# Performance work log

Hardware: AMD Instinct MI355X
Metric: run time of the kernel (lower is better)

The kernel has to match this reference:

```python
import jax, jax.numpy as jnp
import numpy as np

B, S, D, H, W, L, V, FF = 8, 4096, 768, 12, 128, 2, 512, 3072
G_IDX = (0,)


def _ln(x, g, b):
    m = x.mean(-1, keepdims=True)
    v = ((x - m) ** 2).mean(-1, keepdims=True)
    return (x - m) * jax.lax.rsqrt(v + 1e-5) * g + b


def _band_blocks(t, w):
    # t: [B,H,S,Dh] -> key/value blocks [B,H,nb,3w,Dh] (prev/cur/next chunk)
    b, h, s, dh = t.shape
    nb = s // w
    tp = jnp.pad(t, ((0, 0), (0, 0), (w, w), (0, 0))).reshape(b, h, nb + 2, w, dh)
    return jnp.concatenate([tp[:, :, 0:nb], tp[:, :, 1:nb + 1], tp[:, :, 2:nb + 2]], axis=3)


def _longformer_attn(x, att_mask, Wq, bq, Wk, bk, Wv, bv, Wo, bo, w, gidx):
    b, s, d = x.shape
    dh = d // H
    proj = lambda Wm, bm: (x @ Wm.T + bm).reshape(b, s, H, dh).transpose(0, 2, 1, 3)
    q = proj(Wq, bq) / np.float32(np.sqrt(dh))
    k = proj(Wk, bk)
    v = proj(Wv, bv)
    nb = s // w
    qb = q.reshape(b, H, nb, w, dh)
    kb = _band_blocks(k, w)
    vb = _band_blocks(v, w)
    sb = jnp.einsum('bhnqd,bhnkd->bhnqk', qb, kb)  # [B,H,nb,w,3w]
    # window validity: key offset jj relative to query i within chunk
    i = jnp.arange(w)[:, None]
    jj = jnp.arange(3 * w)[None, :]
    allowed = (jj - i >= 0) & (jj - i <= 2 * w)  # [w,3w], |rel pos| <= w
    pos = jnp.arange(nb)[:, None] * w - w + jj  # absolute key positions [nb,3w]
    valid = (pos >= 0) & (pos < s)
    # keys that are global or padded are removed from windowed attention (Longformer)
    key_bias = jnp.where(att_mask != 0, -1e4, 0.0)  # [B,S]
    kbias = jnp.pad(key_bias, ((0, 0), (w, w)), constant_values=-1e9).reshape(b, nb + 2, w)
    kbb = jnp.concatenate([kbias[:, 0:nb], kbias[:, 1:nb + 1], kbias[:, 2:nb + 2]], axis=2)  # [B,nb,3w]
    bias = jnp.where(allowed[None, None] & valid[None, :, None, :], kbb[:, :, None, :], -1e9)
    sb = sb + bias[:, None]  # broadcast over heads
    sb_flat = sb.reshape(b, H, s, 3 * w)
    g = jnp.asarray(gidx)
    ng = g.shape[0]
    kg = k[:, :, g]
    vg = v[:, :, g]
    sg = jnp.einsum('bhsd,bhgd->bhsg', q, kg)  # all queries attend global keys
    probs = jax.nn.softmax(jnp.concatenate([sg, sb_flat], axis=-1), axis=-1)
    pg = probs[..., :ng]
    pb = probs[..., ng:].reshape(b, H, nb, w, 3 * w)
    out = jnp.einsum('bhnqk,bhnkd->bhnqd', pb, vb).reshape(b, H, s, dh)
    out = out + jnp.einsum('bhsg,bhgd->bhsd', pg, vg)
    # global query tokens: full attention over all (non-pad) keys
    qg = q[:, :, g]
    sfull = jnp.einsum('bhgd,bhsd->bhgs', qg, k) + jnp.where(att_mask < 0, -1e4, 0.0)[:, None, None, :]
    og = jnp.einsum('bhgs,bhsd->bhgd', jax.nn.softmax(sfull, axis=-1), v)
    out = out.at[:, :, g].set(og)
    out = out.transpose(0, 2, 1, 3).reshape(b, s, d)
    return out @ Wo.T + bo


def setup_inputs() -> dict:
    key = jax.random.key(0)
    ks = jax.random.split(key, 32)
    sc = 0.02
    inp = {
        'call': jax.random.randint(ks[0], (B, S), 0, V),
        'entry': jax.random.randint(ks[1], (B, S), 0, 2),
        'time': jax.random.randint(ks[2], (B, S), 0, 1000),
        'proc': jax.random.randint(ks[3], (B, S), 0, 64),
        'pid': jax.random.randint(ks[4], (B, S), 0, 64),
        'tid': jax.random.randint(ks[5], (B, S), 0, 64),
        'ret': jax.random.randint(ks[6], (B, S), 0, 2),
        'pad_mask': jnp.zeros((B, S), dtype=bool),
        'chk': 0,
        'emb': jax.random.normal(ks[7], (V, D), jnp.float32) * sc,
        'Wq': jax.random.normal(ks[8], (L, D, D), jnp.float32) * sc,
        'bq': jnp.zeros((L, D), jnp.float32),
        'Wk': jax.random.normal(ks[9], (L, D, D), jnp.float32) * sc,
        'bk': jnp.zeros((L, D), jnp.float32),
        'Wv': jax.random.normal(ks[10], (L, D, D), jnp.float32) * sc,
        'bv': jnp.zeros((L, D), jnp.float32),
        'Wo': jax.random.normal(ks[11], (L, D, D), jnp.float32) * sc,
        'bo': jnp.zeros((L, D), jnp.float32),
        'W1': jax.random.normal(ks[12], (L, FF, D), jnp.float32) * sc,
        'b1': jnp.zeros((L, FF), jnp.float32),
        'W2': jax.random.normal(ks[13], (L, D, FF), jnp.float32) * sc,
        'b2': jnp.zeros((L, D), jnp.float32),
        'g1': jnp.ones((L, D), jnp.float32),
        'beta1': jnp.zeros((L, D), jnp.float32),
        'g2': jnp.ones((L, D), jnp.float32),
        'beta2': jnp.zeros((L, D), jnp.float32),
        'gf': jnp.ones((D,), jnp.float32),
        'betaf': jnp.zeros((D,), jnp.float32),
        'Wc': jax.random.normal(ks[14], (V, D), jnp.float32) * sc,
        'bc': jnp.zeros((V,), jnp.float32),
    }
    return inp


def reference(call, entry, time, proc, pid, tid, ret, pad_mask, chk,
              emb, Wq, bq, Wk, bk, Wv, bv, Wo, bo, W1, b1, W2, b2,
              g1, beta1, g2, beta2, gf, betaf, Wc, bc):
    x = emb[call]  # [B,S,D]; only dim_sys > 0 so embedding == emb_call lookup
    g = jnp.asarray(G_IDX)
    att_mask = jnp.zeros((call.shape[0], call.shape[1]), jnp.float32).at[:, g].set(1e4)
    att_mask = jnp.where(pad_mask, -1e4, att_mask)  # _generate_longformer_mask
    for l in range(L):
        a = _longformer_attn(x, att_mask, Wq[l], bq[l], Wk[l], bk[l], Wv[l], bv[l], Wo[l], bo[l], W, G_IDX)
        x = _ln(x + a, g1[l], beta1[l])
        h = jax.nn.relu(x @ W1[l].T + b1[l]) @ W2[l].T + b2[l]
        x = _ln(x + h, g2[l], beta2[l])
    x = _ln(x, gf, betaf)  # encoder final norm (tfixup=False)
    return x @ Wc.T + bc
```

## Files before the change

kernel.cpp:

```cpp
#include <hip/hip_runtime.h>
#include <hip/hip_bf16.h>
#include <cstddef>
#include <cstdint>

#define Bsz 8
#define Ssz 4096
#define Dsz 768
#define Hh  12
#define Wd  128
#define NBl 32
#define DH  64
#define FFs 3072
#define Vs  512
#define Ls  2
#define GNS 16

typedef __attribute__((ext_vector_type(8))) short short8;
typedef __attribute__((ext_vector_type(4))) float f32x4;

typedef __attribute__((address_space(3))) unsigned short as3_ushort;
typedef __attribute__((address_space(1))) unsigned short as1_ushort;

__device__ inline float b2f(unsigned short u) { union { unsigned int i; float f; } x; x.i = ((unsigned int)u) << 16; return x.f; }
__device__ inline float b2f_lo(unsigned int u) { union { unsigned int i; float f; } x; x.i = (u & 0xffffu) << 16; return x.f; }
__device__ inline float b2f_hi(unsigned int u) { union { unsigned int i; float f; } x; x.i = u & 0xffff0000u; return x.f; }
__device__ inline unsigned short f2bu(float f) {
  __hip_bfloat16 h = __float2bfloat16(f);
  return *reinterpret_cast<unsigned short*>(&h);
}
__device__ inline unsigned int pack2(float lo, float hi) {
  return (unsigned int)f2bu(lo) | ((unsigned int)f2bu(hi) << 16);
}
__device__ inline void glds16(const unsigned short* g, unsigned short* l) {
  __builtin_amdgcn_global_load_lds((const as1_ushort*)g, (as3_ushort*)l, 16, 0, 0);
}

__global__ __launch_bounds__(256) void k_convw(const float* __restrict__ src,
                                               unsigned short* __restrict__ dst, int n) {
  int i8 = (blockIdx.x * 256 + threadIdx.x) * 8;
  if (i8 >= n) return;
  const float4* s4 = reinterpret_cast<const float4*>(src);
  float4 a = s4[i8 >> 2], b = s4[(i8 >> 2) + 1];
  uint4 o;
  o.x = pack2(a.x, a.y); o.y = pack2(a.z, a.w);
  o.z = pack2(b.x, b.y); o.w = pack2(b.z, b.w);
  reinterpret_cast<uint4*>(dst)[i8 >> 3] = o;
}

__global__ __launch_bounds__(256) void k_embed(const int* __restrict__ call,
                                               const float* __restrict__ emb,
                                               unsigned short* __restrict__ x) {
  int idx = blockIdx.x * 256 + threadIdx.x;
  int row = idx / 96;
  int c8  = idx % 96;
  int tok = call[row];
  const float4* s4 = reinterpret_cast<const float4*>(emb + (size_t)tok * Dsz);
  float4 a = s4[c8 * 2], b = s4[c8 * 2 + 1];
  uint4 o;
  o.x = pack2(a.x, a.y); o.y = pack2(a.z, a.w);
  o.z = pack2(b.x, b.y); o.w = pack2(b.z, b.w);
  reinterpret_cast<uint4*>(x)[idx] = o;
}

__global__ __launch_bounds__(256) void k_gemm_lds(
    const unsigned short* __restrict__ A, const unsigned short* __restrict__ Wb,
    const float* __restrict__ bias0, const float* __restrict__ bias1,
    const float* __restrict__ bias2,
    void* __restrict__ o0, void* __restrict__ o1, void* __restrict__ o2,
    int M, int N, int K, int Ng,
    float a0, float a1, float a2, int relu, int out_fp32) {
  __shared__ unsigned short As[128 * 32];
  __shared__ unsigned short Bs[128 * 32];

  const int gx = gridDim.x;
  const int total = gx * (int)gridDim.y;
  const int id = blockIdx.y * gx + blockIdx.x;
  const int swz = (id & 7) * (total >> 3) + (id >> 3);
  const int n0 = (swz % gx) * 128;
  const int m0 = (swz / gx) * 128;

  const int tid  = threadIdx.x;
  const int lane = tid & 63;
  const int wv   = tid >> 6;
  const int wm = wv >> 1, wn = wv & 1;
  const int mr = lane & 15, quad = lane >> 4;

  const int c0 = wv, c1 = wv + 4;
  const int row0 = c0 * 16 + (lane >> 2);
  const int row1 = c1 * 16 + (lane >> 2);
  const int kc0 = (lane & 3) ^ ((row0 >> 1) & 3);
  const int kc1 = (lane & 3) ^ ((row1 >> 1) & 3);
  const unsigned short* gA0 = A  + (size_t)(m0 + row0) * K + kc0 * 8;
  const unsigned short* gA1 = A  + (size_t)(m0 + row1) * K + kc1 * 8;
  const unsigned short* gB0 = Wb + (size_t)(n0 + row0) * K + kc0 * 8;
  const unsigned short* gB1 = Wb + (size_t)(n0 + row1) * K + kc1 * 8;

  int offA[4], offB[4];
#pragma unroll
  for (int mf = 0; mf < 4; mf++) {
    int r = wm * 64 + mf * 16 + mr;
    offA[mf] = r * 32 + ((quad ^ ((r >> 1) & 3)) * 8);
  }
#pragma unroll
  for (int nf = 0; nf < 4; nf++) {
    int r = wn * 64 + nf * 16 + mr;
    offB[nf] = r * 32 + ((quad ^ ((r >> 1) & 3)) * 8);
  }

  f32x4 acc[4][4];
#pragma unroll
  for (int i = 0; i < 4; i++)
#pragma unroll
    for (int j = 0; j < 4; j++) acc[i][j] = (f32x4){0.f, 0.f, 0.f, 0.f};

  for (int k0 = 0; k0 < K; k0 += 32) {
    glds16(gA0 + k0, &As[c0 * 512]);
    glds16(gA1 + k0, &As[c1 * 512]);
    glds16(gB0 + k0, &Bs[c0 * 512]);
    glds16(gB1 + k0, &Bs[c1 * 512]);
    __syncthreads();
    short8 af[4], bf[4];
#pragma unroll
    for (int mf = 0; mf < 4; mf++) af[mf] = *reinterpret_cast<const short8*>(&As[offA[mf]]);
#pragma unroll
    for (int nf = 0; nf < 4; nf++) bf[nf] = *reinterpret_cast<const short8*>(&Bs[offB[nf]]);
#pragma unroll
    for (int mf = 0; mf < 4; mf++)
#pragma unroll
      for (int nf = 0; nf < 4; nf++)
        acc[mf][nf] = __builtin_amdgcn_mfma_f32_16x16x32_bf16(af[mf], bf[nf], acc[mf][nf], 0, 0, 0);
    __syncthreads();
  }

  const int cbase = n0 + wn * 64;
  const int grp = cbase / Ng;
  const float* bp = (grp == 0) ? bias0 : (grp == 1) ? bias1 : bias2;
  const float al = (grp == 0) ? a0 : (grp == 1) ? a1 : a2;
  void* op = (grp == 0) ? o0 : (grp == 1) ? o1 : o2;
  const int colg = cbase - grp * Ng + mr;
#pragma unroll
  for (int nf = 0; nf < 4; nf++) {
    int col = colg + nf * 16;
    float bvv = bp[col];
#pragma unroll
    for (int mf = 0; mf < 4; mf++) {
      int rowb = m0 + wm * 64 + mf * 16 + quad * 4;
#pragma unroll
      for (int r = 0; r < 4; r++) {
        float v = (acc[mf][nf][r] + bvv) * al;
        if (relu) v = fmaxf(v, 0.f);
        if (out_fp32)
          reinterpret_cast<float*>(op)[(size_t)(rowb + r) * Ng + col] = v;
        else
          reinterpret_cast<unsigned short*>(op)[(size_t)(rowb + r) * Ng + col] = f2bu(v);
      }
    }
  }
}


template<int NTT, bool PSEUDO>
__device__ __forceinline__ void chunk_qksm(
    const unsigned short* __restrict__ Ks, unsigned short* __restrict__ Pw,
    const short8 (&qf)[2][2], f32x4 (&o)[2][4],
    float (&mrow)[2][4], float (&lrow)[2][4],
    int RB, int pos0, int relb, int g, int cl) {
  f32x4 S[2][NTT];
#pragma unroll
  for (int mt = 0; mt < 2; mt++)
#pragma unroll
    for (int nt = 0; nt < NTT; nt++) S[mt][nt] = (f32x4){0.f, 0.f, 0.f, 0.f};

  short8 kf[NTT][2];
#pragma unroll
  for (int nt = 0; nt < NTT; nt++) {
    int row = RB + nt * 16 + cl;
    int f2 = (row ^ (row >> 2)) & 7;
#pragma unroll
    for (int ks = 0; ks < 2; ks++)
      kf[nt][ks] = *reinterpret_cast<const short8*>(&Ks[row * 64 + (((ks * 4 + g) ^ f2) << 3)]);
  }
#pragma unroll
  for (int mt = 0; mt < 2; mt++)
#pragma unroll
    for (int nt = 0; nt < NTT; nt++)
#pragma unroll
      for (int ks = 0; ks < 2; ks++)
        S[mt][nt] = __builtin_amdgcn_mfma_f32_16x16x32_bf16(qf[mt][ks], kf[nt][ks], S[mt][nt], 0, 0, 0);

#pragma unroll
  for (int mt = 0; mt < 2; mt++) {
#pragma unroll
    for (int nt = 0; nt < NTT; nt++) {
      int pos = pos0 + nt * 16 + cl;
      bool posok = ((unsigned)pos) < (unsigned)Ssz;
      float pb = (pos == 0) ? -10000.f : 0.f;
#pragma unroll
      for (int r = 0; r < 4; r++) {
        float s = S[mt][nt][r];
        if (PSEUDO) {
          s = (nt == 0 && cl == 0) ? s : -1e30f;
        } else {
          int rel = relb + (nt - mt) * 16 - r;
          s = (posok && ((unsigned)rel <= 256u)) ? (s + pb) : -1e30f;
        }
        S[mt][nt][r] = s;
      }
    }
#pragma unroll
    for (int r = 0; r < 4; r++) {
      float cm = S[mt][0][r];
#pragma unroll
      for (int nt = 1; nt < NTT; nt++) cm = fmaxf(cm, S[mt][nt][r]);
      cm = fmaxf(cm, __shfl_xor(cm, 1));
      cm = fmaxf(cm, __shfl_xor(cm, 2));
      cm = fmaxf(cm, __shfl_xor(cm, 4));
      cm = fmaxf(cm, __shfl_xor(cm, 8));
      float mo = mrow[mt][r];
      float mn = fmaxf(mo, cm);
      float scl = __expf(mo - mn);
      mrow[mt][r] = mn;
      lrow[mt][r] *= scl;
#pragma unroll
      for (int dt = 0; dt < 4; dt++) o[mt][dt][r] *= scl;
      int prow = mt * 16 + g * 4 + r;
      int f2p = (prow ^ (prow >> 2)) & 7;
#pragma unroll
      for (int nt = 0; nt < NTT; nt++) {
        float p = __expf(S[mt][nt][r] - mn);
        lrow[mt][r] += p;
        int pcol = nt * 16 + cl;
        Pw[prow * 64 + (((pcol >> 3) ^ f2p) << 3) + (pcol & 7)] = f2bu(p);
      }
    }
  }
}

template<int KS2>
__device__ __forceinline__ void chunk_pv(
    const unsigned short* __restrict__ Vt, const unsigned short* __restrict__ Pw,
    f32x4 (&o)[2][4], int g, int cl) {
  short8 vf[4][KS2];
#pragma unroll
  for (int dt = 0; dt < 4; dt++) {
    int d = dt * 16 + cl;
    int f2 = (d ^ (d >> 2)) & 7;
#pragma unroll
    for (int ks = 0; ks < KS2; ks++)
      vf[dt][ks] = *reinterpret_cast<const short8*>(&Vt[d * 64 + (((ks * 4 + g) ^ f2) << 3)]);
  }
  short8 pf[2][KS2];
#pragma unroll
  for (int mt = 0; mt < 2; mt++) {
    int prow = mt * 16 + cl;
    int f2 = (prow ^ (prow >> 2)) & 7;
#pragma unroll
    for (int ks = 0; ks < KS2; ks++)
      pf[mt][ks] = *reinterpret_cast<const short8*>(&Pw[prow * 64 + (((ks * 4 + g) ^ f2) << 3)]);
  }
#pragma unroll
  for (int mt = 0; mt < 2; mt++)
#pragma unroll
    for (int dt = 0; dt < 4; dt++)
#pragma unroll
      for (int ks = 0; ks < KS2; ks++)
        o[mt][dt] = __builtin_amdgcn_mfma_f32_16x16x32_bf16(pf[mt][ks], vf[dt][ks], o[mt][dt], 0, 0, 0);
}

__global__ __launch_bounds__(256, 2) void k_band_attn(const unsigned short* __restrict__ K,
                                                      const unsigned short* __restrict__ V,
                                                      unsigned short* __restrict__ Q ) {
  __shared__ unsigned short Ks[416 * 64];
  __shared__ unsigned short Vt[64 * 64];
  __shared__ unsigned short Pb[4][32 * 64];

  const int blk = ((int)blockIdx.x & 7) * 384 + ((int)blockIdx.x >> 3);
  const int n = blk & 31;
  const int h = (blk >> 5) % Hh;
  const int b = blk / (NBl * Hh);
  const int tid = threadIdx.x;
  const int ln = tid & 63;
  const int w = tid >> 6;
  const int g = ln >> 4;
  const int cl = ln & 15;
  const size_t headoff = (size_t)b * Ssz * Dsz + (size_t)h * DH;

#pragma unroll
  for (int it = 0; it < 13; it++) {
    int rb = it * 32 + w * 8;
    int row = rb + (ln >> 3);
    int pos = (row < 384) ? (n - 1) * Wd + row : row - 384;
    pos = pos < 0 ? 0 : (pos > Ssz - 1 ? Ssz - 1 : pos);
    int seg = (ln & 7) ^ ((row ^ (row >> 2)) & 7);
    glds16(K + headoff + (size_t)pos * Dsz + seg * 8, &Ks[rb * 64]);
  }

  short8 qf[2][2];
  {
    const unsigned short* qb = Q + headoff + (size_t)(n * Wd + w * 32 + cl) * Dsz + g * 8;
#pragma unroll
    for (int mt = 0; mt < 2; mt++)
#pragma unroll
      for (int ks = 0; ks < 2; ks++)
        qf[mt][ks] = *reinterpret_cast<const short8*>(qb + (size_t)mt * 16 * Dsz + ks * 32);
  }

  f32x4 o[2][4];
  float mrow[2][4], lrow[2][4];
#pragma unroll
  for (int mt = 0; mt < 2; mt++) {
#pragma unroll
    for (int r = 0; r < 4; r++) { mrow[mt][r] = -1e30f; lrow[mt][r] = 0.f; }
#pragma unroll
    for (int dt = 0; dt < 4; dt++) o[mt][dt] = (f32x4){0.f, 0.f, 0.f, 0.f};
  }

  unsigned short* Pw = &Pb[w][0];
  const int relbase = cl - w * 32 - g * 4;
  const int key0 = 16 * w + (ln >> 3);
  const int dseg = ln & 7;

  uint4 vreg[2];
#pragma unroll
  for (int it = 0; it < 2; it++)
    vreg[it] = *reinterpret_cast<const uint4*>(V + headoff + (size_t)(key0 + it * 8) * Dsz + dseg * 8);

  for (int cc = 0; cc < 7; cc++) {
#pragma unroll
    for (int it = 0; it < 2; it++) {
      int key = key0 + it * 8;
      unsigned int vw_[4] = {vreg[it].x, vreg[it].y, vreg[it].z, vreg[it].w};
#pragma unroll
      for (int j = 0; j < 8; j++) {
        int d = dseg * 8 + j;
        int slot = (key >> 3) ^ ((d ^ (d >> 2)) & 7);
        Vt[d * 64 + (slot << 3) + (key & 7)] = (unsigned short)(vw_[j >> 1] >> ((j & 1) * 16));
      }
    }
    __syncthreads();

    if (cc == 0) {
      chunk_qksm<2, true>(Ks, Pw, qf, o, mrow, lrow, 384, 0, 0, g, cl);
    } else {
      int c = cc - 1;
      chunk_qksm<4, false>(Ks, Pw, qf, o, mrow, lrow, c * 64,
                           (n - 1) * Wd + c * 64, relbase + c * 64, g, cl);
    }

    if (cc < 6) {
      int pos0n = (n - 1) * Wd + cc * 64;
#pragma unroll
      for (int it = 0; it < 2; it++) {
        int pos = pos0n + key0 + it * 8;
        pos = pos < 0 ? 0 : (pos > Ssz - 1 ? Ssz - 1 : pos);
        vreg[it] = *reinterpret_cast<const uint4*>(V + headoff + (size_t)pos * Dsz + dseg * 8);
      }
    }

    if (cc == 0) chunk_pv<1>(Vt, Pw, o, g, cl);
    else         chunk_pv<2>(Vt, Pw, o, g, cl);
    __syncthreads();
  }

#pragma unroll
  for (int mt = 0; mt < 2; mt++)
#pragma unroll
    for (int r = 0; r < 4; r++) {
      float ls = lrow[mt][r];
      ls += __shfl_xor(ls, 1);
      ls += __shfl_xor(ls, 2);
      ls += __shfl_xor(ls, 4);
      ls += __shfl_xor(ls, 8);
      float inv = 1.f / ls;
      int qrow = n * Wd + w * 32 + mt * 16 + g * 4 + r;
      if (qrow != 0) {
        unsigned short* dst = Q + headoff + (size_t)qrow * Dsz;
#pragma unroll
        for (int dt = 0; dt < 4; dt++)
          dst[dt * 16 + cl] = f2bu(o[mt][dt][r] * inv);
      }
    }
}

__global__ __launch_bounds__(256) void k_gattn_part(const unsigned short* __restrict__ K,
                                                    const unsigned short* __restrict__ V,
                                                    const unsigned short* __restrict__ Q,
                                                    float* __restrict__ part) {
  __shared__ float q0[64];
  __shared__ float pj[256];
  __shared__ float red[256];
  const int blk = blockIdx.x;
  const int c = blk & (GNS - 1);
  const int h = (blk / GNS) % Hh;
  const int b = blk / (GNS * Hh);
  const int t = threadIdx.x;
  const size_t base = (size_t)b * Ssz * Dsz + (size_t)h * DH;
  if (t < 64) q0[t] = b2f(Q[base + t]);
  __syncthreads();

  const int j = c * 256 + t;
  const uint4* kp = reinterpret_cast<const uint4*>(K + base + (size_t)j * Dsz);
  float acc = 0.f;
#pragma unroll
  for (int u = 0; u < 8; u++) {
    uint4 w = kp[u];
    acc += q0[u*8+0]*b2f_lo(w.x) + q0[u*8+1]*b2f_hi(w.x)
         + q0[u*8+2]*b2f_lo(w.y) + q0[u*8+3]*b2f_hi(w.y)
         + q0[u*8+4]*b2f_lo(w.z) + q0[u*8+5]*b2f_hi(w.z)
         + q0[u*8+6]*b2f_lo(w.w) + q0[u*8+7]*b2f_hi(w.w);
  }
  red[t] = acc;
  __syncthreads();
  for (int s2 = 128; s2 > 0; s2 >>= 1) {
    if (t < s2) red[t] = fmaxf(red[t], red[t + s2]);
    __syncthreads();
  }
  float m = red[0];
  __syncthreads();
  float p = __expf(acc - m);
  pj[t] = p;
  red[t] = p;
  __syncthreads();
  for (int s2 = 128; s2 > 0; s2 >>= 1) {
    if (t < s2) red[t] += red[t + s2];
    __syncthreads();
  }
  float l = red[0];
  __syncthreads();

  const int d  = t & 63;
  const int gq = t >> 6;
  float oa = 0.f;
  for (int jj = gq * 64; jj < gq * 64 + 64; jj++)
    oa += pj[jj] * b2f(V[base + (size_t)(c * 256 + jj) * Dsz + d]);
  red[t] = oa;
  __syncthreads();

  float* P = part + (size_t)((b * Hh + h) * GNS + c) * 66;
  if (t < 64) P[2 + t] = red[t] + red[64 + t] + red[128 + t] + red[192 + t];
  if (t == 0) { P[0] = m; P[1] = l; }
}

__global__ __launch_bounds__(64) void k_gattn_comb(const float* __restrict__ part,
                                                   unsigned short* __restrict__ Q) {
  const int b = blockIdx.x / Hh;
  const int h = blockIdx.x % Hh;
  const int t = threadIdx.x;
  const float* P = part + (size_t)(b * Hh + h) * GNS * 66;
  float M = -1e30f;
#pragma unroll
  for (int cc = 0; cc < GNS; cc++) M = fmaxf(M, P[cc * 66]);
  float L = 0.f, o = 0.f;
#pragma unroll
  for (int cc = 0; cc < GNS; cc++) {
    float e = __expf(P[cc * 66] - M);
    L += P[cc * 66 + 1] * e;
    o += P[cc * 66 + 2 + t] * e;
  }
  const size_t base = (size_t)b * Ssz * Dsz + (size_t)h * DH;
  Q[base + t] = f2bu(o / L);
}

__global__ __launch_bounds__(256) void k_ln(const unsigned short* __restrict__ x,
                                            const unsigned short* __restrict__ res,
                                            const float* __restrict__ g,
                                            const float* __restrict__ bta,
                                            unsigned short* out) {
  const int row  = blockIdx.x * 4 + (threadIdx.x >> 6);
  const int lane = threadIdx.x & 63;
  const size_t off = (size_t)row * Dsz;
  float v[3][4];
#pragma unroll
  for (int r = 0; r < 3; r++) {
    int d = lane * 4 + r * 256;
    ushort4 xv = *reinterpret_cast<const ushort4*>(x + off + d);
    v[r][0] = b2f(xv.x); v[r][1] = b2f(xv.y);
    v[r][2] = b2f(xv.z); v[r][3] = b2f(xv.w);
    if (res) {
      ushort4 rv = *reinterpret_cast<const ushort4*>(res + off + d);
      v[r][0] += b2f(rv.x); v[r][1] += b2f(rv.y);
      v[r][2] += b2f(rv.z); v[r][3] += b2f(rv.w);
    }
  }
  float s = 0.f;
#pragma unroll
  for (int r = 0; r < 3; r++)
#pragma unroll
    for (int j = 0; j < 4; j++) s += v[r][j];
#pragma unroll
  for (int o2 = 32; o2 > 0; o2 >>= 1) s += __shfl_xor(s, o2);
  float mean = s * (1.f / Dsz);
  float vs = 0.f;
#pragma unroll
  for (int r = 0; r < 3; r++)
#pragma unroll
    for (int j = 0; j < 4; j++) { float dd = v[r][j] - mean; vs += dd * dd; }
#pragma unroll
  for (int o2 = 32; o2 > 0; o2 >>= 1) vs += __shfl_xor(vs, o2);
  float rstd = rsqrtf(vs * (1.f / Dsz) + 1e-5f);
#pragma unroll
  for (int r = 0; r < 3; r++) {
    int d = lane * 4 + r * 256;
    float4 gv = *reinterpret_cast<const float4*>(g + d);
    float4 bv = *reinterpret_cast<const float4*>(bta + d);
    ushort4 ov;
    ov.x = f2bu((v[r][0] - mean) * rstd * gv.x + bv.x);
    ov.y = f2bu((v[r][1] - mean) * rstd * gv.y + bv.y);
    ov.z = f2bu((v[r][2] - mean) * rstd * gv.z + bv.z);
    ov.w = f2bu((v[r][3] - mean) * rstd * gv.w + bv.w);
    *reinterpret_cast<ushort4*>(out + off + d) = ov;
  }
}

static inline unsigned cg8(int n) { return (unsigned)((n / 8 + 255) / 256); }

extern "C" void kernel_launch(void* const* d_in, const int* in_sizes, int n_in,
                              void* d_out, int out_size, void* d_ws, size_t ws_size,
                              hipStream_t stream) {
  const int*   call = (const int*)d_in[0];
  const float* emb  = (const float*)d_in[9];
  const float* Wq = (const float*)d_in[10]; const float* bq = (const float*)d_in[11];
  const float* Wk = (const float*)d_in[12]; const float* bk = (const float*)d_in[13];
  const float* Wv = (const float*)d_in[14]; const float* bv = (const float*)d_in[15];
  const float* Wo = (const float*)d_in[16]; const float* bo = (const float*)d_in[17];
  const float* W1 = (const float*)d_in[18]; const float* b1 = (const float*)d_in[19];
  const float* W2 = (const float*)d_in[20]; const float* b2 = (const float*)d_in[21];
  const float* g1 = (const float*)d_in[22]; const float* bt1 = (const float*)d_in[23];
  const float* g2 = (const float*)d_in[24]; const float* bt2 = (const float*)d_in[25];
  const float* gf = (const float*)d_in[26]; const float* btf = (const float*)d_in[27];
  const float* Wc = (const float*)d_in[28]; const float* bc = (const float*)d_in[29];

  const int DD = Dsz * Dsz;
  const int FD = FFs * Dsz;
  const int M  = Bsz * Ssz;
  const size_t MD = (size_t)M * Dsz;

  unsigned short* ws = (unsigned short*)d_ws;
  unsigned short* X  = ws;
  unsigned short* Qb = X  + MD;
  unsigned short* Kb = Qb + MD;
  unsigned short* Vb = Kb + MD;
  unsigned short* cW = Vb + MD;
  unsigned short* cQKV = cW;
  unsigned short* cWo  = cQKV + (size_t)3 * Ls * DD;
  unsigned short* cW1  = cWo + (size_t)Ls * DD;
  unsigned short* cW2  = cW1 + (size_t)Ls * FD;
  unsigned short* cWc  = cW2 + (size_t)Ls * FD;
  float* gpart = (float*)(cWc + (size_t)Vs * Dsz);
  unsigned short* Hb  = Kb;

  for (int l = 0; l < Ls; l++) {
    k_convw<<<cg8(DD), 256, 0, stream>>>(Wq + (size_t)l*DD, cQKV + (size_t)(l*3+0)*DD, DD);
    k_convw<<<cg8(DD), 256, 0, stream>>>(Wk + (size_t)l*DD, cQKV + (size_t)(l*3+1)*DD, DD);
    k_convw<<<cg8(DD), 256, 0, stream>>>(Wv + (size_t)l*DD, cQKV + (size_t)(l*3+2)*DD, DD);
  }
  k_convw<<<cg8(Ls*DD), 256, 0, stream>>>(Wo, cWo, Ls*DD);
  k_convw<<<cg8(Ls*FD), 256, 0, stream>>>(W1, cW1, Ls*FD);
  k_convw<<<cg8(Ls*FD), 256, 0, stream>>>(W2, cW2, Ls*FD);
  k_convw<<<cg8(Vs*Dsz), 256, 0, stream>>>(Wc, cWc, Vs*Dsz);

  k_embed<<<(unsigned)(M * 96 / 256), 256, 0, stream>>>(call, emb, X);

  for (int l = 0; l < Ls; l++) {
    k_gemm_lds<<<dim3(2304/128, M/128), 256, 0, stream>>>(X, cQKV + (size_t)l*3*DD,
        bq + l*Dsz, bk + l*Dsz, bv + l*Dsz, Qb, Kb, Vb,
        M, 2304, Dsz, Dsz, 0.125f, 1.f, 1.f, 0, 0);
    k_gattn_part<<<Bsz * Hh * GNS, 256, 0, stream>>>(Kb, Vb, Qb, gpart);
    k_band_attn<<<Bsz * Hh * NBl, 256, 0, stream>>>(Kb, Vb, Qb);
    k_gattn_comb<<<Bsz * Hh, 64, 0, stream>>>(gpart, Qb);
    k_gemm_lds<<<dim3(Dsz/128, M/128), 256, 0, stream>>>(Qb, cWo + (size_t)l*DD,
        bo + l*Dsz, bo + l*Dsz, bo + l*Dsz, Kb, Kb, Kb,
        M, Dsz, Dsz, Dsz, 1.f, 1.f, 1.f, 0, 0);
    k_ln<<<M/4, 256, 0, stream>>>(X, Kb, g1 + l*Dsz, bt1 + l*Dsz, X);
    for (int hf = 0; hf < 2; hf++) {
      const size_t mo = (size_t)hf * (M/2);
      k_gemm_lds<<<dim3(FFs/128, (M/2)/128), 256, 0, stream>>>(X + mo*Dsz,
          cW1 + (size_t)l*FD, b1 + l*FFs, b1 + l*FFs, b1 + l*FFs, Hb, Hb, Hb,
          M/2, FFs, Dsz, FFs, 1.f, 1.f, 1.f, 1, 0);
      k_gemm_lds<<<dim3(Dsz/128, (M/2)/128), 256, 0, stream>>>(Hb,
          cW2 + (size_t)l*FD, b2 + l*Dsz, b2 + l*Dsz, b2 + l*Dsz,
          Qb + mo*Dsz, Qb + mo*Dsz, Qb + mo*Dsz,
          M/2, Dsz, FFs, Dsz, 1.f, 1.f, 1.f, 0, 0);
    }
    k_ln<<<M/4, 256, 0, stream>>>(X, Qb, g2 + l*Dsz, bt2 + l*Dsz, X);
  }

  k_ln<<<M/4, 256, 0, stream>>>(X, nullptr, gf, btf, Qb);
  k_gemm_lds<<<dim3(Vs/128, M/128), 256, 0, stream>>>(Qb, cWc,
      bc, bc, bc, (float*)d_out, (float*)d_out, (float*)d_out,
      M, Vs, Dsz, Vs, 1.f, 1.f, 1.f, 0, 1);
}
```

Measured before the change: 2.039 ms.

## Replace 128x128 GEMM with double-buffered 256x256 tile, 512-thread pipelined kernel

Replaces the 128x128x32 single-buffered GEMM with a 256x256x64 tile run by 8 waves. LDS is double-buffered, and the next K-slab's global-to-LDS loads are split into pieces placed between MFMA phases, with raised wave priority during the MFMA blocks. The aim is to cut the global and LDS traffic per FLOP and to hide load latency behind compute. The cost is 128KB of LDS per block, so only one block fits per CU. Larger tiles also mean fewer blocks for the small-N GEMMs (output projection, classifier), which can leave CUs idle.

```diff
diff --git a/kernel.cpp b/kernel.cpp
--- a/kernel.cpp
+++ b/kernel.cpp
@@ -62,74 +62,162 @@
   reinterpret_cast<uint4*>(x)[idx] = o;
 }
 
-__global__ __launch_bounds__(256) void k_gemm_lds(
+__global__ __launch_bounds__(512, 2) void k_gemm256(
     const unsigned short* __restrict__ A, const unsigned short* __restrict__ Wb,
     const float* __restrict__ bias0, const float* __restrict__ bias1,
     const float* __restrict__ bias2,
     void* __restrict__ o0, void* __restrict__ o1, void* __restrict__ o2,
     int M, int N, int K, int Ng,
     float a0, float a1, float a2, int relu, int out_fp32) {
-  __shared__ unsigned short As[128 * 32];
-  __shared__ unsigned short Bs[128 * 32];
+  __shared__ unsigned short As[2][256 * 64];
+  __shared__ unsigned short Bs[2][256 * 64];
 
   const int gx = gridDim.x;
   const int total = gx * (int)gridDim.y;
   const int id = blockIdx.y * gx + blockIdx.x;
   const int swz = (id & 7) * (total >> 3) + (id >> 3);
-  const int n0 = (swz % gx) * 128;
-  const int m0 = (swz / gx) * 128;
-
-  const int tid  = threadIdx.x;
-  const int lane = tid & 63;
-  const int wv   = tid >> 6;
-  const int wm = wv >> 1, wn = wv & 1;
-  const int mr = lane & 15, quad = lane >> 4;
-
-  const int c0 = wv, c1 = wv + 4;
-  const int row0 = c0 * 16 + (lane >> 2);
-  const int row1 = c1 * 16 + (lane >> 2);
-  const int kc0 = (lane & 3) ^ ((row0 >> 1) & 3);
-  const int kc1 = (lane & 3) ^ ((row1 >> 1) & 3);
-  const unsigned short* gA0 = A  + (size_t)(m0 + row0) * K + kc0 * 8;
-  const unsigned short* gA1 = A  + (size_t)(m0 + row1) * K + kc1 * 8;
-  const unsigned short* gB0 = Wb + (size_t)(n0 + row0) * K + kc0 * 8;
-  const unsigned short* gB1 = Wb + (size_t)(n0 + row1) * K + kc1 * 8;
-
-  int offA[4], offB[4];
-#pragma unroll
-  for (int mf = 0; mf < 4; mf++) {
-    int r = wm * 64 + mf * 16 + mr;
-    offA[mf] = r * 32 + ((quad ^ ((r >> 1) & 3)) * 8);
-  }
-#pragma unroll
-  for (int nf = 0; nf < 4; nf++) {
-    int r = wn * 64 + nf * 16 + mr;
-    offB[nf] = r * 32 + ((quad ^ ((r >> 1) & 3)) * 8);
-  }
-
-  f32x4 acc[4][4];
-#pragma unroll
-  for (int i = 0; i < 4; i++)
+  const int n0 = (swz % gx) * 256;
+  const int m0 = (swz / gx) * 256;
+
+  const int tid = threadIdx.x;
+  const int ln = tid & 63;
+  const int w = tid >> 6;
+  const int wm = w >> 2, wn = w & 3;
+  const int mr = ln & 15, quad = ln >> 4;
+
+  const int lr = ln >> 3;
+  const int lc = (ln & 7) ^ lr;
+  const unsigned short* srcA[4];
+  const unsigned short* srcB[4];
+  int ldsOff[4];
+#pragma unroll
+  for (int hi = 0; hi < 2; hi++)
+#pragma unroll
+    for (int i = 0; i < 2; i++) {
+      int r = hi * 128 + (w * 2 + i) * 8;
+      ldsOff[hi * 2 + i] = r * 64;
+      srcA[hi * 2 + i] = A  + (size_t)(m0 + r + lr) * K + lc * 8;
+      srcB[hi * 2 + i] = Wb + (size_t)(n0 + r + lr) * K + lc * 8;
+    }
+
+  const int s0 = (quad ^ (mr & 7)) * 8;
+  const int rowA = wm * 128 + mr;
+  const int rowB = wn * 64 + mr;
+
+  f32x4 acc[8][4];
+#pragma unroll
+  for (int i = 0; i < 8; i++)
 #pragma unroll
     for (int j = 0; j < 4; j++) acc[i][j] = (f32x4){0.f, 0.f, 0.f, 0.f};
 
-  for (int k0 = 0; k0 < K; k0 += 32) {
-    glds16(gA0 + k0, &As[c0 * 512]);
-    glds16(gA1 + k0, &As[c1 * 512]);
-    glds16(gB0 + k0, &Bs[c0 * 512]);
-    glds16(gB1 + k0, &Bs[c1 * 512]);
-    __syncthreads();
-    short8 af[4], bf[4];
-#pragma unroll
-    for (int mf = 0; mf < 4; mf++) af[mf] = *reinterpret_cast<const short8*>(&As[offA[mf]]);
-#pragma unroll
-    for (int nf = 0; nf < 4; nf++) bf[nf] = *reinterpret_cast<const short8*>(&Bs[offB[nf]]);
-#pragma unroll
-    for (int mf = 0; mf < 4; mf++)
-#pragma unroll
-      for (int nf = 0; nf < 4; nf++)
-        acc[mf][nf] = __builtin_amdgcn_mfma_f32_16x16x32_bf16(af[mf], bf[nf], acc[mf][nf], 0, 0, 0);
-    __syncthreads();
+  const int NT = K / 64;
+
+#pragma unroll
+  for (int j = 0; j < 4; j++) glds16(srcA[j], &As[0][ldsOff[j]]);
+#pragma unroll
+  for (int j = 0; j < 4; j++) glds16(srcB[j], &Bs[0][ldsOff[j]]);
+
+  short8 af[4][2];
+  short8 bf[2][2][2];
+
+  for (int t = 0; t < NT; t++) {
+    const int p = t & 1;
+    const unsigned short* Ap = &As[p][0];
+    const unsigned short* Bp = &Bs[p][0];
+    const bool pf = (t + 1 < NT);
+    const int koff = (t + 1) * 64;
+
+    if (pf) {
+      glds16(srcA[0] + koff, &As[p ^ 1][ldsOff[0]]);
+      glds16(srcA[1] + koff, &As[p ^ 1][ldsOff[1]]);
+      asm volatile("s_waitcnt vmcnt(2)" ::: "memory");
+    } else {
+      asm volatile("s_waitcnt vmcnt(0)" ::: "memory");
+    }
+    __builtin_amdgcn_sched_barrier(0);
+    __builtin_amdgcn_s_barrier();
+
+#pragma unroll
+    for (int i = 0; i < 4; i++) {
+      int ro = (rowA + i * 16) * 64;
+      af[i][0] = *reinterpret_cast<const short8*>(&Ap[ro + s0]);
+      af[i][1] = *reinterpret_cast<const short8*>(&Ap[ro + (s0 ^ 32)]);
+    }
+#pragma unroll
+    for (int j = 0; j < 2; j++) {
+      int ro = (rowB + j * 16) * 64;
+      bf[0][j][0] = *reinterpret_cast<const short8*>(&Bp[ro + s0]);
+      bf[0][j][1] = *reinterpret_cast<const short8*>(&Bp[ro + (s0 ^ 32)]);
+    }
+    if (pf) {
+      glds16(srcA[2] + koff, &As[p ^ 1][ldsOff[2]]);
+      glds16(srcA[3] + koff, &As[p ^ 1][ldsOff[3]]);
+    }
+    __builtin_amdgcn_s_setprio(1);
+#pragma unroll
+    for (int i = 0; i < 4; i++)
+#pragma unroll
+      for (int j = 0; j < 2; j++)
+#pragma unroll
+        for (int ks = 0; ks < 2; ks++)
+          acc[i][j] = __builtin_amdgcn_mfma_f32_16x16x32_bf16(af[i][ks], bf[0][j][ks], acc[i][j], 0, 0, 0);
+    __builtin_amdgcn_s_setprio(0);
+    __builtin_amdgcn_s_barrier();
+
+#pragma unroll
+    for (int j = 0; j < 2; j++) {
+      int ro = (rowB + (2 + j) * 16) * 64;
+      bf[1][j][0] = *reinterpret_cast<const short8*>(&Bp[ro + s0]);
+      bf[1][j][1] = *reinterpret_cast<const short8*>(&Bp[ro + (s0 ^ 32)]);
+    }
+    if (pf) {
+      glds16(srcB[0] + koff, &Bs[p ^ 1][ldsOff[0]]);
+      glds16(srcB[1] + koff, &Bs[p ^ 1][ldsOff[1]]);
+    }
+    __builtin_amdgcn_s_setprio(1);
+#pragma unroll
+    for (int i = 0; i < 4; i++)
+#pragma unroll
+      for (int j = 0; j < 2; j++)
+#pragma unroll
+        for (int ks = 0; ks < 2; ks++)
+          acc[i][2 + j] = __builtin_amdgcn_mfma_f32_16x16x32_bf16(af[i][ks], bf[1][j][ks], acc[i][2 + j], 0, 0, 0);
+    __builtin_amdgcn_s_setprio(0);
+    __builtin_amdgcn_s_barrier();
+
+#pragma unroll
+    for (int i = 0; i < 4; i++) {
+      int ro = (rowA + (4 + i) * 16) * 64;
+      af[i][0] = *reinterpret_cast<const short8*>(&Ap[ro + s0]);
+      af[i][1] = *reinterpret_cast<const short8*>(&Ap[ro + (s0 ^ 32)]);
+    }
+    if (pf) {
+      glds16(srcB[2] + koff, &Bs[p ^ 1][ldsOff[2]]);
+      glds16(srcB[3] + koff, &Bs[p ^ 1][ldsOff[3]]);
+    }
+    __builtin_amdgcn_s_setprio(1);
+#pragma unroll
+    for (int i = 0; i < 4; i++)
+#pragma unroll
+      for (int j = 0; j < 2; j++)
+#pragma unroll
+        for (int ks = 0; ks < 2; ks++)
+          acc[4 + i][2 + j] = __builtin_amdgcn_mfma_f32_16x16x32_bf16(af[i][ks], bf[1][j][ks], acc[4 + i][2 + j], 0, 0, 0);
+    __builtin_amdgcn_s_setprio(0);
+    __builtin_amdgcn_s_barrier();
+
+    __builtin_amdgcn_s_setprio(1);
+#pragma unroll
+    for (int i = 0; i < 4; i++)
+#pragma unroll
+      for (int j = 0; j < 2; j++)
+#pragma unroll
+        for (int ks = 0; ks < 2; ks++)
+          acc[4 + i][j] = __builtin_amdgcn_mfma_f32_16x16x32_bf16(af[i][ks], bf[0][j][ks], acc[4 + i][j], 0, 0, 0);
+    __builtin_amdgcn_s_setprio(0);
+    asm volatile("s_waitcnt lgkmcnt(0)" ::: "memory");
+    __builtin_amdgcn_sched_barrier(0);
+    __builtin_amdgcn_s_barrier();
   }
 
   const int cbase = n0 + wn * 64;
@@ -140,19 +228,18 @@
   const int colg = cbase - grp * Ng + mr;
 #pragma unroll
   for (int nf = 0; nf < 4; nf++) {
-    int col = colg + nf * 16;
-    float bvv = bp[col];
-#pragma unroll
-    for (int mf = 0; mf < 4; mf++) {
-      int rowb = m0 + wm * 64 + mf * 16 + quad * 4;
+    float bv = bp[colg + nf * 16];
+#pragma unroll
+    for (int mf = 0; mf < 8; mf++) {
+      int rowb = m0 + wm * 128 + mf * 16 + quad * 4;
 #pragma unroll
       for (int r = 0; r < 4; r++) {
-        float v = (acc[mf][nf][r] + bvv) * al;
+        float v = (acc[mf][nf][r] + bv) * al;
         if (relu) v = fmaxf(v, 0.f);
         if (out_fp32)
-          reinterpret_cast<float*>(op)[(size_t)(rowb + r) * Ng + col] = v;
+          reinterpret_cast<float*>(op)[(size_t)(rowb + r) * Ng + colg + nf * 16] = v;
         else
-          reinterpret_cast<unsigned short*>(op)[(size_t)(rowb + r) * Ng + col] = f2bu(v);
+          reinterpret_cast<unsigned short*>(op)[(size_t)(rowb + r) * Ng + colg + nf * 16] = f2bu(v);
       }
     }
   }
@@ -562,22 +649,22 @@
   k_embed<<<(unsigned)(M * 96 / 256), 256, 0, stream>>>(call, emb, X);
 
   for (int l = 0; l < Ls; l++) {
-    k_gemm_lds<<<dim3(2304/128, M/128), 256, 0, stream>>>(X, cQKV + (size_t)l*3*DD,
+    k_gemm256<<<dim3(2304/256, M/256), 512, 0, stream>>>(X, cQKV + (size_t)l*3*DD,
         bq + l*Dsz, bk + l*Dsz, bv + l*Dsz, Qb, Kb, Vb,
         M, 2304, Dsz, Dsz, 0.125f, 1.f, 1.f, 0, 0);
     k_gattn_part<<<Bsz * Hh * GNS, 256, 0, stream>>>(Kb, Vb, Qb, gpart);
     k_band_attn<<<Bsz * Hh * NBl, 256, 0, stream>>>(Kb, Vb, Qb);
     k_gattn_comb<<<Bsz * Hh, 64, 0, stream>>>(gpart, Qb);
-    k_gemm_lds<<<dim3(Dsz/128, M/128), 256, 0, stream>>>(Qb, cWo + (size_t)l*DD,
+    k_gemm256<<<dim3(Dsz/256, M/256), 512, 0, stream>>>(Qb, cWo + (size_t)l*DD,
         bo + l*Dsz, bo + l*Dsz, bo + l*Dsz, Kb, Kb, Kb,
         M, Dsz, Dsz, Dsz, 1.f, 1.f, 1.f, 0, 0);
     k_ln<<<M/4, 256, 0, stream>>>(X, Kb, g1 + l*Dsz, bt1 + l*Dsz, X);
     for (int hf = 0; hf < 2; hf++) {
       const size_t mo = (size_t)hf * (M/2);
-      k_gemm_lds<<<dim3(FFs/128, (M/2)/128), 256, 0, stream>>>(X + mo*Dsz,
+      k_gemm256<<<dim3(FFs/256, (M/2)/256), 512, 0, stream>>>(X + mo*Dsz,
           cW1 + (size_t)l*FD, b1 + l*FFs, b1 + l*FFs, b1 + l*FFs, Hb, Hb, Hb,
           M/2, FFs, Dsz, FFs, 1.f, 1.f, 1.f, 1, 0);
-      k_gemm_lds<<<dim3(Dsz/128, (M/2)/128), 256, 0, stream>>>(Hb,
+      k_gemm256<<<dim3(Dsz/256, (M/2)/256), 512, 0, stream>>>(Hb,
           cW2 + (size_t)l*FD, b2 + l*Dsz, b2 + l*Dsz, b2 + l*Dsz,
           Qb + mo*Dsz, Qb + mo*Dsz, Qb + mo*Dsz,
           M/2, Dsz, FFs, Dsz, 1.f, 1.f, 1.f, 0, 0);
@@ -586,7 +673,7 @@
   }
 
   k_ln<<<M/4, 256, 0, stream>>>(X, nullptr, gf, btf, Qb);
-  k_gemm_lds<<<dim3(Vs/128, M/128), 256, 0, stream>>>(Qb, cWc,
+  k_gemm256<<<dim3(Vs/256, M/256), 512, 0, stream>>>(Qb, cWc,
       bc, bc, bc, (float*)d_out, (float*)d_out, (float*)d_out,
       M, Vs, Dsz, Vs, 1.f, 1.f, 1.f, 0, 1);
 }
```

Result: faster. 1.925 ms (-5.6%).
